# Kernel tuning notes

Measured on AMD Instinct MI355X. Metric: run time of the kernel, lower is better.

Reference implementation:

```python
import jax, jax.numpy as jnp
import numpy as np

RADIUS = 4.0
NSAMPLE = 8
NUM_SAMPLES = 64  # hard-coded in furthest_point_sample(coor, 64)
EPS = 1e-5
DIM = 256


def fps_single(coor):
    N = coor.shape[0]
    def step(carry, _):
        dists, last = carry
        d = jnp.sum((coor - coor[last]) ** 2, axis=-1)
        dists = jnp.minimum(dists, d)
        nxt = jnp.argmax(dists).astype(jnp.int32)
        return (dists, nxt), nxt
    init = (jnp.full((N,), 1e10, dtype=coor.dtype), jnp.int32(0))
    _, idxs = jax.lax.scan(step, init, None, length=NUM_SAMPLES - 1)
    return jnp.concatenate([jnp.zeros((1,), jnp.int32), idxs])


def ball_query_single(coor, centers):
    # coor [N,3], centers [S,3] -> [S,NSAMPLE] first-nsample-in-index-order within radius,
    # padded with the first valid index (pointnet2 ball_query semantics)
    N = coor.shape[0]
    d2 = jnp.sum((centers[:, None, :] - coor[None, :, :]) ** 2, axis=-1)  # [S,N]
    valid = d2 < RADIUS * RADIUS
    cand = jnp.where(valid, jnp.arange(N, dtype=jnp.int32)[None, :], N)
    idx = jnp.sort(cand, axis=1)[:, :NSAMPLE]
    first = idx[:, :1]  # center itself is always within radius -> always valid
    return jnp.where(idx == N, first, idx)


def layer_norm(x, g, b):
    m = jnp.mean(x, axis=-1, keepdims=True)
    v = jnp.var(x, axis=-1, keepdims=True)
    return (x - m) / jnp.sqrt(v + EPS) * g + b


def cross_attn(q, k, v, Wq, Wk):
    # num_heads=1, no qk scaling (qk_scale is never applied in the torch code)
    qh = q @ Wq.T                # [B,S,C]
    kh = k @ Wk.T                # [B,S,C]
    attn = jax.nn.softmax(jnp.einsum('bnc,bmc->bnm', qh, kh), axis=-1)
    return jnp.einsum('bnm,bmd->bnd', attn, v)  # [B,S,3]


def reference(input_feature, x, coor, Wq, Wk, gq, bq, gk, bk):
    B, N, C = x.shape
    S = NUM_SAMPLES
    idx = jax.vmap(fps_single)(coor)                                   # [B,S]
    sample_coor = jnp.take_along_axis(coor, idx[..., None], axis=1)    # [B,S,3]
    sample_x = jnp.take_along_axis(x, idx[..., None], axis=1)          # [B,S,C]
    sample_if = jnp.take_along_axis(input_feature, idx[..., None], axis=1)

    nidx = jax.vmap(ball_query_single)(coor, sample_coor)              # [B,S,ns]
    gather = jax.vmap(lambda a, i: a[i])                               # [B,S,ns,D]
    g_coor = gather(coor, nidx) - sample_coor[:, :, None, :]           # relative xyz
    g_x = gather(x, nidx)
    g_if = gather(input_feature, nidx)

    diff_if = jnp.mean(g_if, axis=2)      # [B,S,3]
    diff_coor = jnp.mean(g_coor, axis=2)  # [B,S,3]
    global_x = jnp.max(g_x, axis=2)       # [B,S,C]
    x_2 = global_x - sample_x             # [B,S,C]

    # torch does v.view(B, NK, 1, -1) on a contiguous [B,3,S] tensor -> raw reshape,
    # NOT a transpose; replicate exactly
    v_coor = jnp.transpose(diff_coor, (0, 2, 1)).reshape(B, S, 3)
    v_if = jnp.transpose(diff_if, (0, 2, 1)).reshape(B, S, 3)

    nk = layer_norm(sample_x, gk, bk)
    nq = layer_norm(x_2, gq, bq)
    coor_2 = cross_attn(nq, nk, v_coor, Wq, Wk)
    if_2 = cross_attn(nq, nk, v_if, Wq, Wk)

    return (sample_x + x_2, sample_coor + coor_2, sample_if + if_2)


def setup_inputs() -> dict:
    key = jax.random.key(0)
    ks = jax.random.split(key, 8)
    B, N = 16, 32768
    return {
        'input_feature': jax.random.normal(ks[0], (B, N, 3), jnp.float32),
        'x': jax.random.normal(ks[1], (B, N, DIM), jnp.float32),
        'coor': jax.random.normal(ks[2], (B, N, 3), jnp.float32),
        'Wq': jax.random.normal(ks[3], (DIM, DIM), jnp.float32) * 0.02,
        'Wk': jax.random.normal(ks[4], (DIM, DIM), jnp.float32) * 0.02,
        'gq': jnp.ones((DIM,), jnp.float32),
        'bq': jnp.zeros((DIM,), jnp.float32),
        'gk': jnp.ones((DIM,), jnp.float32),
        'bk': jnp.zeros((DIM,), jnp.float32),
    }
```

## Files before the change

### kernel.cpp

```cpp
#include <hip/hip_runtime.h>
#include <hip/hip_bf16.h>

#define N_PTS 32768
#define NB    16
#define NS    64
#define DIMC  256

__global__ __launch_bounds__(1024) void fps_kernel(const float* __restrict__ coor,
                                                   int* __restrict__ idx_out) {
  __shared__ float4 s_d4[N_PTS / 4];
  __shared__ float  s_rv[16];
  __shared__ int    s_ri[16];
  __shared__ float  s_c[3];
  const int b = blockIdx.x;
  const int t = threadIdx.x;
  const float* __restrict__ C = coor + (size_t)b * N_PTS * 3;

  float px[32], py[32], pz[32];
#pragma unroll
  for (int g = 0; g < 8; ++g) {
#pragma unroll
    for (int k = 0; k < 4; ++k) {
      const int p = g * 4096 + t * 4 + k;
      px[g * 4 + k] = C[p * 3 + 0];
      py[g * 4 + k] = C[p * 3 + 1];
      pz[g * 4 + k] = C[p * 3 + 2];
    }
    s_d4[g * 1024 + t] = make_float4(1e10f, 1e10f, 1e10f, 1e10f);
  }
  if (t == 0) {
    idx_out[b * NS] = 0;
    s_c[0] = C[0]; s_c[1] = C[1]; s_c[2] = C[2];
  }
  __syncthreads();

  for (int step = 1; step < NS; ++step) {
    const float cx = s_c[0], cy = s_c[1], cz = s_c[2];
    float bestv = -1.0f;
    int   besti = 0;
#pragma unroll
    for (int g = 0; g < 8; ++g) {
      const float4 od = s_d4[g * 1024 + t];
      float nd[4];
      const int pb = g * 4096 + t * 4;
#pragma unroll
      for (int k = 0; k < 4; ++k) {
        const float dx = __fsub_rn(px[g * 4 + k], cx);
        const float dy = __fsub_rn(py[g * 4 + k], cy);
        const float dz = __fsub_rn(pz[g * 4 + k], cz);
        const float d  = __fadd_rn(__fadd_rn(__fmul_rn(dx, dx), __fmul_rn(dy, dy)),
                                   __fmul_rn(dz, dz));
        const float o  = (k == 0) ? od.x : (k == 1) ? od.y : (k == 2) ? od.z : od.w;
        nd[k] = fminf(o, d);
      }
      s_d4[g * 1024 + t] = make_float4(nd[0], nd[1], nd[2], nd[3]);
#pragma unroll
      for (int k = 0; k < 4; ++k) {
        if (nd[k] > bestv) { bestv = nd[k]; besti = pb + k; }
      }
    }
#pragma unroll
    for (int off = 32; off >= 1; off >>= 1) {
      const float ov = __shfl_down(bestv, off);
      const int   oi = __shfl_down(besti, off);
      if (ov > bestv || (ov == bestv && oi < besti)) { bestv = ov; besti = oi; }
    }
    if ((t & 63) == 0) { s_rv[t >> 6] = bestv; s_ri[t >> 6] = besti; }
    __syncthreads();
    if (t == 0) {
      float bv = s_rv[0]; int bi = s_ri[0];
      for (int w = 1; w < 16; ++w) {
        const float v = s_rv[w]; const int i2 = s_ri[w];
        if (v > bv || (v == bv && i2 < bi)) { bv = v; bi = i2; }
      }
      idx_out[b * NS + step] = bi;
      s_c[0] = C[bi * 3 + 0]; s_c[1] = C[bi * 3 + 1]; s_c[2] = C[bi * 3 + 2];
    }
    __syncthreads();
  }
}

__global__ __launch_bounds__(64) void neigh_kernel(
    const float* __restrict__ coor, const float* __restrict__ x,
    const float* __restrict__ infeat, const int* __restrict__ idx,
    const float* __restrict__ gq, const float* __restrict__ bq,
    const float* __restrict__ gk, const float* __restrict__ bk,
    float* __restrict__ nq, float* __restrict__ nk, float* __restrict__ stats,
    float* __restrict__ out0) {
  const int bs = blockIdx.x;
  const int b  = bs >> 6;
  const int t  = threadIdx.x;
  const float* __restrict__ C = coor   + (size_t)b * N_PTS * 3;
  const float* __restrict__ X = x      + (size_t)b * N_PTS * DIMC;
  const float* __restrict__ F = infeat + (size_t)b * N_PTS * 3;
  int ci = idx[bs];
  ci = __builtin_amdgcn_readfirstlane(ci);
  const float cx = C[ci * 3 + 0], cy = C[ci * 3 + 1], cz = C[ci * 3 + 2];

  __shared__ int s_nidx[8];
  int found = 0;
  for (int base = 0; base < N_PTS && found < 8; base += 64) {
    const int p = base + t;
    const float dx = __fsub_rn(C[p * 3 + 0], cx);
    const float dy = __fsub_rn(C[p * 3 + 1], cy);
    const float dz = __fsub_rn(C[p * 3 + 2], cz);
    const float d2 = __fadd_rn(__fadd_rn(__fmul_rn(dx, dx), __fmul_rn(dy, dy)),
                               __fmul_rn(dz, dz));
    const bool valid = d2 < 16.0f;
    const unsigned long long m = __ballot(valid);
    if (valid) {
      const int slot = found + (int)__popcll(m & ((1ull << t) - 1ull));
      if (slot < 8) s_nidx[slot] = p;
    }
    found += (int)__popcll(m);
  }
  __syncthreads();
  if (t == 0) {
    const int total = found < 8 ? found : 8;
    for (int k = total; k < 8; ++k) s_nidx[k] = s_nidx[0];
  }
  __syncthreads();

  float ax = 0, ay = 0, az = 0, fx = 0, fy = 0, fz = 0;
  if (t < 8) {
    const int n = s_nidx[t];
    ax = C[n * 3 + 0]; ay = C[n * 3 + 1]; az = C[n * 3 + 2];
    fx = F[n * 3 + 0]; fy = F[n * 3 + 1]; fz = F[n * 3 + 2];
  }
#pragma unroll
  for (int off = 4; off >= 1; off >>= 1) {
    ax += __shfl_down(ax, off); ay += __shfl_down(ay, off); az += __shfl_down(az, off);
    fx += __shfl_down(fx, off); fy += __shfl_down(fy, off); fz += __shfl_down(fz, off);
  }
  if (t == 0) {
    float* dco = stats;
    float* dif = stats + 3072;
    float* sco = stats + 6144;
    float* sif = stats + 9216;
    dco[bs * 3 + 0] = ax * 0.125f - cx;
    dco[bs * 3 + 1] = ay * 0.125f - cy;
    dco[bs * 3 + 2] = az * 0.125f - cz;
    dif[bs * 3 + 0] = fx * 0.125f;
    dif[bs * 3 + 1] = fy * 0.125f;
    dif[bs * 3 + 2] = fz * 0.125f;
    sco[bs * 3 + 0] = cx; sco[bs * 3 + 1] = cy; sco[bs * 3 + 2] = cz;
    sif[bs * 3 + 0] = F[ci * 3 + 0];
    sif[bs * 3 + 1] = F[ci * 3 + 1];
    sif[bs * 3 + 2] = F[ci * 3 + 2];
  }

  const int c0 = t * 4;
  int nn[8];
#pragma unroll
  for (int k = 0; k < 8; ++k) nn[k] = s_nidx[k];
  float4 g = *(const float4*)(X + (size_t)nn[0] * DIMC + c0);
#pragma unroll
  for (int k = 1; k < 8; ++k) {
    const float4 rr = *(const float4*)(X + (size_t)nn[k] * DIMC + c0);
    g.x = fmaxf(g.x, rr.x); g.y = fmaxf(g.y, rr.y);
    g.z = fmaxf(g.z, rr.z); g.w = fmaxf(g.w, rr.w);
  }
  const float4 sx = *(const float4*)(X + (size_t)ci * DIMC + c0);

  *(float4*)(out0 + (size_t)bs * DIMC + c0) = g;

  const float4 x2 = make_float4(g.x - sx.x, g.y - sx.y, g.z - sx.z, g.w - sx.w);

  float s1 = x2.x + x2.y + x2.z + x2.w;
  float s2 = x2.x * x2.x + x2.y * x2.y + x2.z * x2.z + x2.w * x2.w;
  float u1 = sx.x + sx.y + sx.z + sx.w;
  float u2 = sx.x * sx.x + sx.y * sx.y + sx.z * sx.z + sx.w * sx.w;
#pragma unroll
  for (int off = 1; off < 64; off <<= 1) {
    s1 += __shfl_xor(s1, off); s2 += __shfl_xor(s2, off);
    u1 += __shfl_xor(u1, off); u2 += __shfl_xor(u2, off);
  }
  const float mq = s1 * (1.0f / 256.0f);
  const float vq = s2 * (1.0f / 256.0f) - mq * mq;
  const float rq = 1.0f / sqrtf(vq + 1e-5f);
  const float mk = u1 * (1.0f / 256.0f);
  const float vk = u2 * (1.0f / 256.0f) - mk * mk;
  const float rk = 1.0f / sqrtf(vk + 1e-5f);

  const float4 gqv = *(const float4*)(gq + c0);
  const float4 bqv = *(const float4*)(bq + c0);
  const float4 gkv = *(const float4*)(gk + c0);
  const float4 bkv = *(const float4*)(bk + c0);

  float4 nqv = make_float4((x2.x - mq) * rq * gqv.x + bqv.x,
                           (x2.y - mq) * rq * gqv.y + bqv.y,
                           (x2.z - mq) * rq * gqv.z + bqv.z,
                           (x2.w - mq) * rq * gqv.w + bqv.w);
  float4 nkv = make_float4((sx.x - mk) * rk * gkv.x + bkv.x,
                           (sx.y - mk) * rk * gkv.y + bkv.y,
                           (sx.z - mk) * rk * gkv.z + bkv.z,
                           (sx.w - mk) * rk * gkv.w + bkv.w);
  *(float4*)(nq + (size_t)bs * DIMC + c0) = nqv;
  *(float4*)(nk + (size_t)bs * DIMC + c0) = nkv;
}

__global__ __launch_bounds__(256) void wqwk_kernel(const float* __restrict__ Wq,
                                                   const float* __restrict__ Wk,
                                                   float* __restrict__ M) {
  const int i0 = blockIdx.x * 16;
  const int j  = threadIdx.x;
  float acc[16];
#pragma unroll
  for (int ii = 0; ii < 16; ++ii) acc[ii] = 0.0f;
  for (int c = 0; c < 256; ++c) {
    const float wk = Wk[c * 256 + j];
#pragma unroll
    for (int ii = 0; ii < 16; ++ii) acc[ii] = fmaf(Wq[c * 256 + i0 + ii], wk, acc[ii]);
  }
#pragma unroll
  for (int ii = 0; ii < 16; ++ii) M[(i0 + ii) * 256 + j] = acc[ii];
}

__global__ __launch_bounds__(256) void kt_kernel(const float* __restrict__ nk,
                                                 const float* __restrict__ M,
                                                 float* __restrict__ kt) {
  __shared__ float lnk[64 * 256];
  const int b  = blockIdx.x >> 3;
  const int it = blockIdx.x & 7;
  const int t  = threadIdx.x;
  const float* __restrict__ NK = nk + (size_t)b * NS * DIMC;
  for (int r = 0; r < 64; ++r) lnk[r * 256 + ((t + r) & 255)] = NK[r * 256 + t];
  __syncthreads();

  const int rr = t & 63;
  const int ig = t >> 6;
  const int i0 = it * 32 + ig * 8;
  float acc[8];
#pragma unroll
  for (int k = 0; k < 8; ++k) acc[k] = 0.0f;
  for (int j = 0; j < 256; ++j) {
    const float v = lnk[rr * 256 + ((j + rr) & 255)];
#pragma unroll
    for (int k = 0; k < 8; ++k) acc[k] = fmaf(M[(i0 + k) * 256 + j], v, acc[k]);
  }
#pragma unroll
  for (int k = 0; k < 8; ++k) kt[((size_t)b * NS + rr) * DIMC + i0 + k] = acc[k];
}

__global__ __launch_bounds__(256) void attn_kernel(const float* __restrict__ nq,
                                                   const float* __restrict__ ktm,
                                                   const float* __restrict__ stats,
                                                   float* __restrict__ out1,
                                                   float* __restrict__ out2) {
  const int blk = blockIdx.x;
  const int b = blk >> 2, rg = blk & 3, t = threadIdx.x;
  const int rl = t >> 4, r = rg * 16 + rl, m0 = (t & 15) * 4;
  const float4* __restrict__ Q = (const float4*)(nq  + ((size_t)b * NS + r)  * DIMC);
  const float4* __restrict__ K = (const float4*)(ktm + ((size_t)b * NS + m0) * DIMC);
  float a0 = 0, a1 = 0, a2 = 0, a3 = 0;
  for (int j = 0; j < 64; ++j) {
    const float4 q  = Q[j];
    const float4 k0 = K[j];
    const float4 k1 = K[j + 64];
    const float4 k2 = K[j + 128];
    const float4 k3 = K[j + 192];
    a0 += q.x * k0.x + q.y * k0.y + q.z * k0.z + q.w * k0.w;
    a1 += q.x * k1.x + q.y * k1.y + q.z * k1.z + q.w * k1.w;
    a2 += q.x * k2.x + q.y * k2.y + q.z * k2.z + q.w * k2.w;
    a3 += q.x * k3.x + q.y * k3.y + q.z * k3.z + q.w * k3.w;
  }
  float mx = fmaxf(fmaxf(a0, a1), fmaxf(a2, a3));
#pragma unroll
  for (int off = 1; off < 16; off <<= 1) mx = fmaxf(mx, __shfl_xor(mx, off, 16));
  const float e0 = expf(a0 - mx), e1 = expf(a1 - mx), e2 = expf(a2 - mx), e3 = expf(a3 - mx);
  float sm = e0 + e1 + e2 + e3;
#pragma unroll
  for (int off = 1; off < 16; off <<= 1) sm += __shfl_xor(sm, off, 16);
  const float inv = 1.0f / sm;
  float pr[4] = {e0 * inv, e1 * inv, e2 * inv, e3 * inv};

  const float* dco = stats;
  const float* dif = stats + 3072;
  const float* sco = stats + 6144;
  const float* sif = stats + 9216;
#pragma unroll
  for (int c = 0; c < 3; ++c) {
    float oc = 0, oi = 0;
#pragma unroll
    for (int mm = 0; mm < 4; ++mm) {
      const int q3 = 3 * (m0 + mm) + c;
      const int row = q3 & 63, col = q3 >> 6;
      oc = fmaf(pr[mm], dco[((size_t)b * NS + row) * 3 + col], oc);
      oi = fmaf(pr[mm], dif[((size_t)b * NS + row) * 3 + col], oi);
    }
#pragma unroll
    for (int off = 1; off < 16; off <<= 1) {
      oc += __shfl_xor(oc, off, 16);
      oi += __shfl_xor(oi, off, 16);
    }
    if ((t & 15) == 0) {
      const size_t o = ((size_t)b * NS + r) * 3 + c;
      out1[o] = sco[o] + oc;
      out2[o] = sif[o] + oi;
    }
  }
}

extern "C" void kernel_launch(void* const* d_in, const int* in_sizes, int n_in,
                              void* d_out, int out_size, void* d_ws, size_t ws_size,
                              hipStream_t stream) {
  const float* infeat = (const float*)d_in[0];
  const float* x      = (const float*)d_in[1];
  const float* coor   = (const float*)d_in[2];
  const float* Wq     = (const float*)d_in[3];
  const float* Wk     = (const float*)d_in[4];
  const float* gq     = (const float*)d_in[5];
  const float* bq     = (const float*)d_in[6];
  const float* gk     = (const float*)d_in[7];
  const float* bk     = (const float*)d_in[8];

  float* out0 = (float*)d_out;
  float* out1 = out0 + (size_t)NB * NS * DIMC;
  float* out2 = out1 + (size_t)NB * NS * 3;

  char* ws = (char*)d_ws;
  int*   idx   = (int*)(ws);
  float* nq    = (float*)(ws + 4096);
  float* nk    = (float*)(ws + 4096 + (1u << 20));
  float* ktw   = (float*)(ws + 4096 + (2u << 20));
  float* M     = (float*)(ws + 4096 + (3u << 20));
  float* stats = (float*)(ws + 4096 + (3u << 20) + (256u << 10));

  fps_kernel<<<NB, 1024, 0, stream>>>(coor, idx);
  wqwk_kernel<<<16, 256, 0, stream>>>(Wq, Wk, M);
  neigh_kernel<<<NB * NS, 64, 0, stream>>>(coor, x, infeat, idx, gq, bq, gk, bk,
                                           nq, nk, stats, out0);
  kt_kernel<<<128, 256, 0, stream>>>(nk, M, ktw);
  attn_kernel<<<64, 256, 0, stream>>>(nq, ktw, stats, out1, out2);
}
```

Measured before the change: 1.144 ms.

## Keep FPS distances in registers, move z to LDS, use 512-thread blocks

The FPS kernel now runs 512 threads per block, each handling 64 points. The running min-distance array moves from shared memory into registers, while the z coordinates move into shared memory. Coordinate loads are vectorised as float4, and the final cross-wave reduction uses shuffles instead of a serial loop on one thread. The aim is to cut per-step LDS read/write traffic and shorten the serial reduction in this latency-bound loop, at the cost of higher register pressure (64 × 3 floats per thread) and fewer waves per block.

```diff
diff --git a/kernel.cpp b/kernel.cpp
--- a/kernel.cpp
+++ b/kernel.cpp
@@ -6,27 +6,30 @@
 #define NS    64
 #define DIMC  256
 
-__global__ __launch_bounds__(1024) void fps_kernel(const float* __restrict__ coor,
-                                                   int* __restrict__ idx_out) {
-  __shared__ float4 s_d4[N_PTS / 4];
-  __shared__ float  s_rv[16];
-  __shared__ int    s_ri[16];
+__global__ __launch_bounds__(512, 2) void fps_kernel(const float* __restrict__ coor,
+                                                     int* __restrict__ idx_out) {
+  __shared__ float4 s_pz[16 * 512];
+  __shared__ float  s_rv[8];
+  __shared__ int    s_ri[8];
   __shared__ float  s_c[3];
   const int b = blockIdx.x;
   const int t = threadIdx.x;
   const float* __restrict__ C = coor + (size_t)b * N_PTS * 3;
 
-  float px[32], py[32], pz[32];
-#pragma unroll
-  for (int g = 0; g < 8; ++g) {
-#pragma unroll
-    for (int k = 0; k < 4; ++k) {
-      const int p = g * 4096 + t * 4 + k;
-      px[g * 4 + k] = C[p * 3 + 0];
-      py[g * 4 + k] = C[p * 3 + 1];
-      pz[g * 4 + k] = C[p * 3 + 2];
-    }
-    s_d4[g * 1024 + t] = make_float4(1e10f, 1e10f, 1e10f, 1e10f);
+  float px[64], py[64], d[64];
+#pragma unroll
+  for (int g = 0; g < 16; ++g) {
+    const int p0 = g * 2048 + t * 4;
+    const float4 c0 = *(const float4*)(C + (size_t)p0 * 3);
+    const float4 c1 = *(const float4*)(C + (size_t)p0 * 3 + 4);
+    const float4 c2 = *(const float4*)(C + (size_t)p0 * 3 + 8);
+    px[g * 4 + 0] = c0.x; py[g * 4 + 0] = c0.y;
+    px[g * 4 + 1] = c0.w; py[g * 4 + 1] = c1.x;
+    px[g * 4 + 2] = c1.z; py[g * 4 + 2] = c1.w;
+    px[g * 4 + 3] = c2.y; py[g * 4 + 3] = c2.z;
+    s_pz[g * 512 + t] = make_float4(c0.z, c1.y, c2.x, c2.w);
+    d[g * 4 + 0] = 1e10f; d[g * 4 + 1] = 1e10f;
+    d[g * 4 + 2] = 1e10f; d[g * 4 + 3] = 1e10f;
   }
   if (t == 0) {
     idx_out[b * NS] = 0;
@@ -39,24 +42,20 @@
     float bestv = -1.0f;
     int   besti = 0;
 #pragma unroll
-    for (int g = 0; g < 8; ++g) {
-      const float4 od = s_d4[g * 1024 + t];
-      float nd[4];
-      const int pb = g * 4096 + t * 4;
+    for (int g = 0; g < 16; ++g) {
+      const float4 pz4 = s_pz[g * 512 + t];
+      const int pb = g * 2048 + t * 4;
 #pragma unroll
       for (int k = 0; k < 4; ++k) {
+        const float pz = (k == 0) ? pz4.x : (k == 1) ? pz4.y : (k == 2) ? pz4.z : pz4.w;
         const float dx = __fsub_rn(px[g * 4 + k], cx);
         const float dy = __fsub_rn(py[g * 4 + k], cy);
-        const float dz = __fsub_rn(pz[g * 4 + k], cz);
-        const float d  = __fadd_rn(__fadd_rn(__fmul_rn(dx, dx), __fmul_rn(dy, dy)),
+        const float dz = __fsub_rn(pz, cz);
+        const float dd = __fadd_rn(__fadd_rn(__fmul_rn(dx, dx), __fmul_rn(dy, dy)),
                                    __fmul_rn(dz, dz));
-        const float o  = (k == 0) ? od.x : (k == 1) ? od.y : (k == 2) ? od.z : od.w;
-        nd[k] = fminf(o, d);
-      }
-      s_d4[g * 1024 + t] = make_float4(nd[0], nd[1], nd[2], nd[3]);
-#pragma unroll
-      for (int k = 0; k < 4; ++k) {
-        if (nd[k] > bestv) { bestv = nd[k]; besti = pb + k; }
+        const float nd = fminf(d[g * 4 + k], dd);
+        d[g * 4 + k] = nd;
+        if (nd > bestv) { bestv = nd; besti = pb + k; }
       }
     }
 #pragma unroll
@@ -67,14 +66,19 @@
     }
     if ((t & 63) == 0) { s_rv[t >> 6] = bestv; s_ri[t >> 6] = besti; }
     __syncthreads();
-    if (t == 0) {
-      float bv = s_rv[0]; int bi = s_ri[0];
-      for (int w = 1; w < 16; ++w) {
-        const float v = s_rv[w]; const int i2 = s_ri[w];
-        if (v > bv || (v == bv && i2 < bi)) { bv = v; bi = i2; }
+    if (t < 64) {
+      float v = (t < 8) ? s_rv[t] : -1.0f;
+      int   i = (t < 8) ? s_ri[t] : 0x7fffffff;
+#pragma unroll
+      for (int off = 4; off >= 1; off >>= 1) {
+        const float ov = __shfl_down(v, off);
+        const int   oi = __shfl_down(i, off);
+        if (ov > v || (ov == v && oi < i)) { v = ov; i = oi; }
       }
-      idx_out[b * NS + step] = bi;
-      s_c[0] = C[bi * 3 + 0]; s_c[1] = C[bi * 3 + 1]; s_c[2] = C[bi * 3 + 2];
+      if (t == 0) {
+        idx_out[b * NS + step] = i;
+        s_c[0] = C[i * 3 + 0]; s_c[1] = C[i * 3 + 1]; s_c[2] = C[i * 3 + 2];
+      }
     }
     __syncthreads();
   }
@@ -326,7 +330,7 @@
   float* M     = (float*)(ws + 4096 + (3u << 20));
   float* stats = (float*)(ws + 4096 + (3u << 20) + (256u << 10));
 
-  fps_kernel<<<NB, 1024, 0, stream>>>(coor, idx);
+  fps_kernel<<<NB, 512, 0, stream>>>(coor, idx);
   wqwk_kernel<<<16, 256, 0, stream>>>(Wq, Wk, M);
   neigh_kernel<<<NB * NS, 64, 0, stream>>>(coor, x, infeat, idx, gq, bq, gk, bk,
                                            nq, nk, stats, out0);
```

Measured after the change: 1.036 ms. 1.1x faster.
